# Optimization experiments

Hardware: AMD Instinct MI355X
Metric: run time of the kernel (lower is better)

The kernel has to match this reference:

```python
import jax, jax.numpy as jnp
import numpy as np

C = 256
EPS = 1e-5


def dwconv3x3(x, w):
    # x: [B,C,H,W], w: [C,1,3,3] depthwise (groups=C)
    return jax.lax.conv_general_dilated(
        x, w, window_strides=(1, 1), padding=((1, 1), (1, 1)),
        dimension_numbers=('NCHW', 'OIHW', 'NCHW'), feature_group_count=x.shape[1])


def bn(x, gamma, beta, mean, var):
    # inference-mode batchnorm over channel dim of NCHW
    inv = gamma * jax.lax.rsqrt(var + EPS)
    return x * inv[:, None, None] + (beta - mean * inv)[:, None, None]


def setup_inputs() -> dict:
    key = jax.random.key(0)
    ks = jax.random.split(key, 8)
    B, H, W = 32, 64, 64
    inp = {
        'x': jax.random.normal(ks[0], (B, C, H, W), jnp.float32),
        'edge_w': jax.random.normal(ks[1], (C, 1, 3, 3), jnp.float32) * 0.1,
        'edge_gamma': jnp.ones((C,), jnp.float32),
        'edge_beta': jnp.zeros((C,), jnp.float32),
        'edge_mean': jnp.zeros((C,), jnp.float32),
        'edge_var': jnp.ones((C,), jnp.float32),
        'fc1_w': jax.random.normal(ks[2], (C // 16, C), jnp.float32) * 0.05,
        'fc2_w': jax.random.normal(ks[3], (C, C // 16), jnp.float32) * 0.05,
        'fusion_w': jax.random.normal(ks[4], (C, 2 * C), jnp.float32) * 0.05,
        'fusion_b': jnp.zeros((C,), jnp.float32),
        'bn1_gamma': jnp.ones((C,), jnp.float32),
        'bn1_beta': jnp.zeros((C,), jnp.float32),
        'bn1_mean': jnp.zeros((C,), jnp.float32),
        'bn1_var': jnp.ones((C,), jnp.float32),
        'deform_w': jax.random.normal(ks[5], (C, 1, 3, 3), jnp.float32) * 0.1,
        'balance_w': jax.random.normal(ks[6], (C, C), jnp.float32) * 0.05,
        'balance_b': jnp.zeros((C,), jnp.float32),
        'bn2_gamma': jnp.ones((C,), jnp.float32),
        'bn2_beta': jnp.zeros((C,), jnp.float32),
        'bn2_mean': jnp.zeros((C,), jnp.float32),
        'bn2_var': jnp.ones((C,), jnp.float32),
    }
    return inp


def reference(x, edge_w, edge_gamma, edge_beta, edge_mean, edge_var,
              fc1_w, fc2_w, fusion_w, fusion_b,
              bn1_gamma, bn1_beta, bn1_mean, bn1_var,
              deform_w, balance_w, balance_b,
              bn2_gamma, bn2_beta, bn2_mean, bn2_var):
    # --- EdgeEnhancementAttention ---
    edge = jax.nn.relu(bn(dwconv3x3(x, edge_w), edge_gamma, edge_beta, edge_mean, edge_var))
    # SE channel attention
    avg = jnp.mean(x, axis=(2, 3))                       # [B,C]
    att = jax.nn.relu(avg @ fc1_w.T)                     # [B,C/16]
    att = jax.nn.sigmoid(att @ fc2_w.T)                  # [B,C]
    enhanced = x * att[:, :, None, None]
    fused = jnp.concatenate([enhanced, edge], axis=1)    # [B,2C,H,W]
    out = jnp.einsum('bchw,oc->bohw', fused, fusion_w) + fusion_b[None, :, None, None]
    out = bn(out, bn1_gamma, bn1_beta, bn1_mean, bn1_var)
    # --- DeformConv2d with zero offsets == plain depthwise 3x3 conv, no bias ---
    out = dwconv3x3(out, deform_w)
    # --- balance: 1x1 conv + BN, then gate by input ---
    out = jnp.einsum('bchw,oc->bohw', out, balance_w) + balance_b[None, :, None, None]
    out = bn(out, bn2_gamma, bn2_beta, bn2_mean, bn2_var)
    return out * x
```

## Files before the change

kernel.cpp:

```cpp
#include <hip/hip_runtime.h>
#include <math.h>

#define HW 4096
#define PLSTRIDE ((size_t)HW * 8)

typedef unsigned short ushort_t;
typedef short v8s __attribute__((ext_vector_type(8)));
typedef float v4f __attribute__((ext_vector_type(4)));

__device__ __forceinline__ float bf2f(ushort_t u) {
    union { unsigned int i; float f; } v; v.i = ((unsigned int)u) << 16; return v.f;
}
__device__ __forceinline__ ushort_t f2bf(float f) {
    unsigned int x = __float_as_uint(f);
    x += 0x7fffu + ((x >> 16) & 1u);
    return (ushort_t)(x >> 16);
}

__device__ __forceinline__ void gld16(const ushort_t* g, ushort_t* l) {
    __builtin_amdgcn_global_load_lds(
        (__attribute__((address_space(1))) void*)g,
        (__attribute__((address_space(3))) void*)l, 16, 0, 0);
}

__global__ __launch_bounds__(256) void k_consts(
    const float* eg, const float* ebt, const float* em, const float* ev,
    const float* fb,
    const float* g1, const float* b1, const float* m1, const float* v1,
    const float* balb,
    const float* g2, const float* b2, const float* m2, const float* v2,
    float* cbuf)
{
    int c = threadIdx.x;
    float iE = eg[c] * rsqrtf(ev[c] + 1e-5f);
    cbuf[c]       = iE;
    cbuf[256 + c] = ebt[c] - em[c] * iE;
    float i1 = g1[c] * rsqrtf(v1[c] + 1e-5f);
    cbuf[512 + c] = i1;
    cbuf[768 + c] = b1[c] - m1[c] * i1 + fb[c] * i1;
    float i2 = g2[c] * rsqrtf(v2[c] + 1e-5f);
    cbuf[1024 + c] = i2;
    cbuf[1280 + c] = b2[c] - m2[c] * i2 + balb[c] * i2;
}

__global__ __launch_bounds__(256) void k_wcopy(const float* fusw, const float* balw,
                                               ushort_t* fusw2b, ushort_t* balwb)
{
    int o = blockIdx.x, t = threadIdx.x;
    fusw2b[o * 256 + t] = f2bf(fusw[o * 512 + 256 + t]);
    balwb[o * 256 + t]  = f2bf(balw[o * 256 + t]);
}

__global__ __launch_bounds__(512) void k_edge(const float* x, const float* ew,
                                              const float* cbuf, ushort_t* A,
                                              float* avg)
{
    __shared__ __align__(16) ushort_t Xs[4096];
    __shared__ __align__(16) ushort_t Es[4096];
    int cg = blockIdx.x;
    int b = blockIdx.y;
    int t = threadIdx.x;
    int w = t & 63;
    int pl = t >> 6;
    int c = cg * 8 + pl;
    const float* px = x + ((size_t)(b * 256 + c)) * HW;
    ushort_t* AX = A + ((size_t)(b * 64 + cg)) * PLSTRIDE;
    ushort_t* AE = A + ((size_t)(b * 64 + 32 + cg)) * PLSTRIDE;
    float wt[9];
    #pragma unroll
    for (int k = 0; k < 9; ++k) wt[k] = ew[c * 9 + k];
    float sE = cbuf[c], cE = cbuf[256 + c];
    bool wl = (w > 0), wrr = (w < 63);

    float p0l = 0.f, p0c = 0.f, p0r = 0.f;
    float p1l, p1c, p1r;
    p1c = px[w];
    p1l = wl ? px[w - 1] : 0.f;
    p1r = wrr ? px[w + 1] : 0.f;
    float s = 0.f;
    for (int hb = 0; hb < 8; ++hb) {
        #pragma unroll
        for (int hi = 0; hi < 8; ++hi) {
            int h = hb * 8 + hi;
            float p2l, p2c, p2r;
            if (h < 63) {
                const float* row = px + (h + 1) * 64;
                p2c = row[w];
                p2l = wl ? row[w - 1] : 0.f;
                p2r = wrr ? row[w + 1] : 0.f;
            } else {
                p2l = p2c = p2r = 0.f;
            }
            float a = p0l * wt[0] + p0c * wt[1] + p0r * wt[2]
                    + p1l * wt[3] + p1c * wt[4] + p1r * wt[5]
                    + p2l * wt[6] + p2c * wt[7] + p2r * wt[8];
            s += p1c;
            float v = a * sE + cE;
            Es[hi * 512 + w * 8 + pl] = f2bf(v > 0.f ? v : 0.f);
            Xs[hi * 512 + w * 8 + pl] = f2bf(p1c);
            p0l = p1l; p0c = p1c; p0r = p1r;
            p1l = p2l; p1c = p2c; p1r = p2r;
        }
        __syncthreads();
        {
            int hwg = (hb * 8 + pl) * 64 + w;
            uint4 vx = *(const uint4*)&Xs[pl * 512 + w * 8];
            uint4 ve = *(const uint4*)&Es[pl * 512 + w * 8];
            *(uint4*)(AX + (size_t)hwg * 8) = vx;
            *(uint4*)(AE + (size_t)hwg * 8) = ve;
        }
        __syncthreads();
    }
    #pragma unroll
    for (int off = 32; off > 0; off >>= 1) s += __shfl_down(s, off, 64);
    if ((t & 63) == 0) avg[b * 256 + c] = s * (1.0f / HW);
}

__global__ __launch_bounds__(256) void k_sefold(const float* avg, const float* fc1,
                                                const float* fc2, const float* fusw,
                                                ushort_t* w1b)
{
    int b = blockIdx.x, t = threadIdx.x;
    __shared__ float av[256];
    __shared__ float hid[16];
    av[t] = avg[b * 256 + t];
    __syncthreads();
    if (t < 16) {
        float h = 0.f;
        for (int c = 0; c < 256; ++c) h += av[c] * fc1[t * 256 + c];
        hid[t] = h > 0.f ? h : 0.f;
    }
    __syncthreads();
    float a = 0.f;
    #pragma unroll
    for (int j = 0; j < 16; ++j) a += hid[j] * fc2[t * 16 + j];
    float att = 1.0f / (1.0f + expf(-a));
    ushort_t* wout = w1b + (size_t)b * 65536;
    for (int o = 0; o < 256; ++o)
        wout[o * 256 + t] = f2bf(fusw[o * 512 + t] * att);
}

__global__ __launch_bounds__(512, 4) void k_gemm1(ushort_t* __restrict__ A,
                                                  const ushort_t* __restrict__ w1b,
                                                  const ushort_t* __restrict__ fusw2b,
                                                  const float* __restrict__ cbuf)
{
    __shared__ __align__(16) ushort_t At[128 * 64];
    __shared__ __align__(16) ushort_t Bt[256 * 64];
    int bid = blockIdx.x;
    int orig = (bid & 7) * 128 + (bid >> 3);
    int b = orig >> 5;
    int hw0 = (orig & 31) * 128;
    int t = threadIdx.x;
    int lane = t & 63, wv = t >> 6;
    int quad = lane >> 4, l16 = lane & 15;
    int wr = wv >> 2, wc = wv & 3;
    int srow = lane >> 3, kch = lane & 7;

    v4f acc[4][4];
    #pragma unroll
    for (int i = 0; i < 4; ++i)
        #pragma unroll
        for (int j = 0; j < 4; ++j) acc[i][j] = (v4f){0.f, 0.f, 0.f, 0.f};

    for (int kb = 0; kb < 8; ++kb) {
        __syncthreads();
        #pragma unroll
        for (int r = 0; r < 2; ++r) {
            int mrow = wv * 8 + r * 64 + srow;
            int csw = kch ^ (mrow & 7);
            gld16(A + ((size_t)(b * 64 + kb * 8 + csw)) * PLSTRIDE
                    + (size_t)(hw0 + mrow) * 8,
                  &At[(wv * 8 + r * 64) * 64]);
        }
        #pragma unroll
        for (int r = 0; r < 4; ++r) {
            int orow = wv * 8 + r * 64 + srow;
            int kc2 = kch ^ (orow & 7);
            const ushort_t* bs = (kb < 4)
                ? (w1b + ((size_t)(b * 256 + orow)) * 256 + kb * 64 + kc2 * 8)
                : (fusw2b + ((size_t)orow) * 256 + (kb - 4) * 64 + kc2 * 8);
            gld16(bs, &Bt[(wv * 8 + r * 64) * 64]);
        }
        __syncthreads();
        #pragma unroll
        for (int ks2 = 0; ks2 < 2; ++ks2) {
            v8s afr[4], bfr[4];
            #pragma unroll
            for (int mt = 0; mt < 4; ++mt) {
                int ml = wr * 64 + mt * 16 + l16;
                int jj = (ks2 * 4 + quad) ^ (ml & 7);
                afr[mt] = *(const v8s*)(&At[ml * 64 + jj * 8]);
            }
            #pragma unroll
            for (int nt = 0; nt < 4; ++nt) {
                int ol = wc * 64 + nt * 16 + l16;
                int jj = (ks2 * 4 + quad) ^ (ol & 7);
                bfr[nt] = *(const v8s*)(&Bt[ol * 64 + jj * 8]);
            }
            #pragma unroll
            for (int mt = 0; mt < 4; ++mt)
                #pragma unroll
                for (int nt = 0; nt < 4; ++nt)
                    acc[mt][nt] = __builtin_amdgcn_mfma_f32_16x16x32_bf16(
                        afr[mt], bfr[nt], acc[mt][nt], 0, 0, 0);
        }
    }

    #pragma unroll
    for (int nt = 0; nt < 4; ++nt) {
        int o = wc * 64 + nt * 16 + l16;
        float s1 = cbuf[512 + o], c1 = cbuf[768 + o];
        ushort_t* op = A + ((size_t)(b * 64 + 32 + (o >> 3))) * PLSTRIDE + (o & 7);
        #pragma unroll
        for (int mt = 0; mt < 4; ++mt)
            #pragma unroll
            for (int r = 0; r < 4; ++r) {
                int m = hw0 + wr * 64 + mt * 16 + quad * 4 + r;
                op[(size_t)m * 8] = f2bf(acc[mt][nt][r] * s1 + c1);
            }
    }
}

__global__ __launch_bounds__(256) void k_dw2(ushort_t* __restrict__ A,
                                             const float* __restrict__ dfw)
{
    int t = threadIdx.x;
    int w = t & 63;
    int pl = t >> 6;
    int cg = blockIdx.x * 4 + pl;
    int b = blockIdx.y;
    int h0 = blockIdx.z * 32;
    const ushort_t* pE = A + ((size_t)(b * 64 + 32 + cg)) * PLSTRIDE;
    ushort_t* pX = A + ((size_t)(b * 64 + cg)) * PLSTRIDE;
    float wt[3][3][8];
    #pragma unroll
    for (int r = 0; r < 3; ++r)
        #pragma unroll
        for (int d = 0; d < 3; ++d)
            #pragma unroll
            for (int ch = 0; ch < 8; ++ch)
                wt[r][d][ch] = dfw[(cg * 8 + ch) * 9 + r * 3 + d];
    bool wl = (w > 0), wrr = (w < 63);

    uint4 rm, rc, rp;
    rm = (h0 > 0) ? *(const uint4*)(pE + (size_t)((h0 - 1) * 64 + w) * 8)
                  : (uint4){0u, 0u, 0u, 0u};
    rc = *(const uint4*)(pE + (size_t)(h0 * 64 + w) * 8);

#define DWROW(v, r) { \
    unsigned int cx0 = v.x, cx1 = v.y, cx2 = v.z, cx3 = v.w; \
    unsigned int lx0 = __shfl_up(cx0, 1, 64), lx1 = __shfl_up(cx1, 1, 64); \
    unsigned int lx2 = __shfl_up(cx2, 1, 64), lx3 = __shfl_up(cx3, 1, 64); \
    unsigned int rx0 = __shfl_down(cx0, 1, 64), rx1 = __shfl_down(cx1, 1, 64); \
    unsigned int rx2 = __shfl_down(cx2, 1, 64), rx3 = __shfl_down(cx3, 1, 64); \
    unsigned int cw[4] = { cx0, cx1, cx2, cx3 }; \
    unsigned int lw[4] = { lx0, lx1, lx2, lx3 }; \
    unsigned int rw[4] = { rx0, rx1, rx2, rx3 }; \
    _Pragma("unroll") for (int ch = 0; ch < 8; ++ch) { \
        float fC = bf2f((ch & 1) ? (ushort_t)(cw[ch >> 1] >> 16) \
                                 : (ushort_t)(cw[ch >> 1] & 0xffff)); \
        float fL = wl ? bf2f((ch & 1) ? (ushort_t)(lw[ch >> 1] >> 16) \
                                      : (ushort_t)(lw[ch >> 1] & 0xffff)) : 0.f; \
        float fR = wrr ? bf2f((ch & 1) ? (ushort_t)(rw[ch >> 1] >> 16) \
                                       : (ushort_t)(rw[ch >> 1] & 0xffff)) : 0.f; \
        acc[ch] += fL * wt[r][0][ch] + fC * wt[r][1][ch] + fR * wt[r][2][ch]; \
    } }

    for (int s = 0; s < 32; ++s) {
        int h = h0 + s;
        rp = (h + 1 < 64) ? *(const uint4*)(pE + (size_t)((h + 1) * 64 + w) * 8)
                          : (uint4){0u, 0u, 0u, 0u};
        float acc[8];
        #pragma unroll
        for (int ch = 0; ch < 8; ++ch) acc[ch] = 0.f;
        DWROW(rm, 0);
        DWROW(rc, 1);
        DWROW(rp, 2);
        uint4 ov;
        ov.x = (unsigned int)f2bf(acc[0]) | ((unsigned int)f2bf(acc[1]) << 16);
        ov.y = (unsigned int)f2bf(acc[2]) | ((unsigned int)f2bf(acc[3]) << 16);
        ov.z = (unsigned int)f2bf(acc[4]) | ((unsigned int)f2bf(acc[5]) << 16);
        ov.w = (unsigned int)f2bf(acc[6]) | ((unsigned int)f2bf(acc[7]) << 16);
        *(uint4*)(pX + (size_t)(h * 64 + w) * 8) = ov;
        rm = rc; rc = rp;
    }
#undef DWROW
}

__global__ __launch_bounds__(512, 4) void k_gemm2(ushort_t* __restrict__ A,
                                                  const ushort_t* __restrict__ balwb)
{
    __shared__ __align__(16) ushort_t At[128 * 64];
    __shared__ __align__(16) ushort_t Bt[256 * 64];
    int bid = blockIdx.x;
    int orig = (bid & 7) * 128 + (bid >> 3);
    int b = orig >> 5;
    int hw0 = (orig & 31) * 128;
    int t = threadIdx.x;
    int lane = t & 63, wv = t >> 6;
    int quad = lane >> 4, l16 = lane & 15;
    int wr = wv >> 2, wc = wv & 3;
    int srow = lane >> 3, kch = lane & 7;

    v4f acc[4][4];
    #pragma unroll
    for (int i = 0; i < 4; ++i)
        #pragma unroll
        for (int j = 0; j < 4; ++j) acc[i][j] = (v4f){0.f, 0.f, 0.f, 0.f};

    for (int kb = 0; kb < 4; ++kb) {
        __syncthreads();
        #pragma unroll
        for (int r = 0; r < 2; ++r) {
            int mrow = wv * 8 + r * 64 + srow;
            int csw = kch ^ (mrow & 7);
            gld16(A + ((size_t)(b * 64 + kb * 8 + csw)) * PLSTRIDE
                    + (size_t)(hw0 + mrow) * 8,
                  &At[(wv * 8 + r * 64) * 64]);
        }
        #pragma unroll
        for (int r = 0; r < 4; ++r) {
            int orow = wv * 8 + r * 64 + srow;
            int kc2 = kch ^ (orow & 7);
            gld16(balwb + ((size_t)orow) * 256 + kb * 64 + kc2 * 8,
                  &Bt[(wv * 8 + r * 64) * 64]);
        }
        __syncthreads();
        #pragma unroll
        for (int ks2 = 0; ks2 < 2; ++ks2) {
            v8s afr[4], bfr[4];
            #pragma unroll
            for (int mt = 0; mt < 4; ++mt) {
                int ml = wr * 64 + mt * 16 + l16;
                int jj = (ks2 * 4 + quad) ^ (ml & 7);
                afr[mt] = *(const v8s*)(&At[ml * 64 + jj * 8]);
            }
            #pragma unroll
            for (int nt = 0; nt < 4; ++nt) {
                int ol = wc * 64 + nt * 16 + l16;
                int jj = (ks2 * 4 + quad) ^ (ol & 7);
                bfr[nt] = *(const v8s*)(&Bt[ol * 64 + jj * 8]);
            }
            #pragma unroll
            for (int mt = 0; mt < 4; ++mt)
                #pragma unroll
                for (int nt = 0; nt < 4; ++nt)
                    acc[mt][nt] = __builtin_amdgcn_mfma_f32_16x16x32_bf16(
                        afr[mt], bfr[nt], acc[mt][nt], 0, 0, 0);
        }
    }

    #pragma unroll
    for (int nt = 0; nt < 4; ++nt) {
        int o = wc * 64 + nt * 16 + l16;
        ushort_t* op = A + ((size_t)(b * 64 + 32 + (o >> 3))) * PLSTRIDE + (o & 7);
        #pragma unroll
        for (int mt = 0; mt < 4; ++mt)
            #pragma unroll
            for (int r = 0; r < 4; ++r) {
                int m = hw0 + wr * 64 + mt * 16 + quad * 4 + r;
                op[(size_t)m * 8] = f2bf(acc[mt][nt][r]);
            }
    }
}

__global__ __launch_bounds__(256) void k_final(const ushort_t* A, const float* x,
                                               const float* cbuf, float* out)
{
    __shared__ float Lt[64 * 65];
    int bid = blockIdx.x;
    int b = bid >> 8;
    int rem = bid & 255;
    int hw0 = (rem >> 2) * 64;
    int c0 = (rem & 3) * 64;
    int t = threadIdx.x;
    #pragma unroll
    for (int r = 0; r < 2; ++r) {
        int idx = r * 256 + t;
        int cq = idx >> 6;
        int hwl = idx & 63;
        uint4 v = *(const uint4*)(A + ((size_t)(b * 64 + 32 + (c0 >> 3) + cq)) * PLSTRIDE
                                    + (size_t)(hw0 + hwl) * 8);
        unsigned int wd[4] = { v.x, v.y, v.z, v.w };
        #pragma unroll
        for (int j = 0; j < 8; ++j) {
            ushort_t u = (j & 1) ? (ushort_t)(wd[j >> 1] >> 16) : (ushort_t)(wd[j >> 1] & 0xffff);
            Lt[(cq * 8 + j) * 65 + hwl] = bf2f(u);
        }
    }
    __syncthreads();
    int hw_l = t & 63;
    int c_l0 = t >> 6;
    #pragma unroll
    for (int j = 0; j < 16; ++j) {
        int c_l = c_l0 * 16 + j;
        int c = c0 + c_l;
        float s2 = cbuf[1024 + c], c2 = cbuf[1280 + c];
        size_t g = ((size_t)b * 256 + c) * HW + hw0 + hw_l;
        float xv = x[g];
        out[g] = (Lt[c_l * 65 + hw_l] * s2 + c2) * xv;
    }
}

extern "C" void kernel_launch(void* const* d_in, const int* in_sizes, int n_in,
                              void* d_out, int out_size, void* d_ws, size_t ws_size,
                              hipStream_t stream)
{
    const float* x    = (const float*)d_in[0];
    const float* ew   = (const float*)d_in[1];
    const float* fc1  = (const float*)d_in[6];
    const float* fc2  = (const float*)d_in[7];
    const float* fusw = (const float*)d_in[8];
    const float* dfw  = (const float*)d_in[14];
    const float* balw = (const float*)d_in[15];
    float* out = (float*)d_out;

    char* ws = (char*)d_ws;
    ushort_t* A      = (ushort_t*)(ws);
    ushort_t* w1b    = (ushort_t*)(ws + 134217728);
    ushort_t* fusw2b = (ushort_t*)(ws + 138412032);
    ushort_t* balwb  = (ushort_t*)(ws + 138543104);
    float*    avg    = (float*)(ws + 138674176);
    float*    cbuf   = (float*)(ws + 138706944);

    k_consts<<<1, 256, 0, stream>>>((const float*)d_in[2], (const float*)d_in[3],
                                    (const float*)d_in[4], (const float*)d_in[5],
                                    (const float*)d_in[9],
                                    (const float*)d_in[10], (const float*)d_in[11],
                                    (const float*)d_in[12], (const float*)d_in[13],
                                    (const float*)d_in[16],
                                    (const float*)d_in[17], (const float*)d_in[18],
                                    (const float*)d_in[19], (const float*)d_in[20],
                                    cbuf);
    k_wcopy<<<256, 256, 0, stream>>>(fusw, balw, fusw2b, balwb);
    k_edge<<<dim3(32, 32), 512, 0, stream>>>(x, ew, cbuf, A, avg);
    k_sefold<<<32, 256, 0, stream>>>(avg, fc1, fc2, fusw, w1b);
    k_gemm1<<<1024, 512, 0, stream>>>(A, w1b, fusw2b, cbuf);
    k_dw2<<<dim3(8, 32, 2), 256, 0, stream>>>(A, dfw);
    k_gemm2<<<1024, 512, 0, stream>>>(A, balwb);
    k_final<<<8192, 256, 0, stream>>>(A, x, cbuf, out);
}
```

Before: 538.5 us.

## Vectorize edge kernel with float4 row loads, lane shuffles, and swizzled LDS transpose

The depthwise edge kernel now has each lane load float4 vectors covering four columns of three rows, taking the horizontal neighbours from adjacent lanes with shuffles instead of issuing scalar per-column loads. Results are packed as bf16 pairs into a 16-row XOR-swizzled LDS tile and transposed into the channel-interleaved layout with wider stores. Barriers drop from 16 to 8 per block. The goal is fewer global load instructions, fewer LDS bank conflicts and fewer synchronisations, at the cost of redundant vertical-neighbour loads and extra pack/unpack ALU work.

```diff
diff --git a/kernel.cpp b/kernel.cpp
--- a/kernel.cpp
+++ b/kernel.cpp
@@ -55,13 +55,16 @@
                                               const float* cbuf, ushort_t* A,
                                               float* avg)
 {
-    __shared__ __align__(16) ushort_t Xs[4096];
-    __shared__ __align__(16) ushort_t Es[4096];
+    __shared__ unsigned int Xs[16][8][32];
+    __shared__ unsigned int Es[16][8][32];
     int cg = blockIdx.x;
     int b = blockIdx.y;
     int t = threadIdx.x;
-    int w = t & 63;
+    int lane = t & 63;
     int pl = t >> 6;
+    int q = lane >> 4;
+    int l16 = lane & 15;
+    int w4 = l16 * 4;
     int c = cg * 8 + pl;
     const float* px = x + ((size_t)(b * 256 + c)) * HW;
     ushort_t* AX = A + ((size_t)(b * 64 + cg)) * PLSTRIDE;
@@ -70,44 +73,90 @@
     #pragma unroll
     for (int k = 0; k < 9; ++k) wt[k] = ew[c * 9 + k];
     float sE = cbuf[c], cE = cbuf[256 + c];
-    bool wl = (w > 0), wrr = (w < 63);
-
-    float p0l = 0.f, p0c = 0.f, p0r = 0.f;
-    float p1l, p1c, p1r;
-    p1c = px[w];
-    p1l = wl ? px[w - 1] : 0.f;
-    p1r = wrr ? px[w + 1] : 0.f;
+    bool wlz = (l16 > 0), wrz = (l16 < 15);
     float s = 0.f;
-    for (int hb = 0; hb < 8; ++hb) {
-        #pragma unroll
-        for (int hi = 0; hi < 8; ++hi) {
-            int h = hb * 8 + hi;
-            float p2l, p2c, p2r;
-            if (h < 63) {
-                const float* row = px + (h + 1) * 64;
-                p2c = row[w];
-                p2l = wl ? row[w - 1] : 0.f;
-                p2r = wrr ? row[w + 1] : 0.f;
-            } else {
-                p2l = p2c = p2r = 0.f;
-            }
-            float a = p0l * wt[0] + p0c * wt[1] + p0r * wt[2]
-                    + p1l * wt[3] + p1c * wt[4] + p1r * wt[5]
-                    + p2l * wt[6] + p2c * wt[7] + p2r * wt[8];
-            s += p1c;
-            float v = a * sE + cE;
-            Es[hi * 512 + w * 8 + pl] = f2bf(v > 0.f ? v : 0.f);
-            Xs[hi * 512 + w * 8 + pl] = f2bf(p1c);
-            p0l = p1l; p0c = p1c; p0r = p1r;
-            p1l = p2l; p1c = p2c; p1r = p2r;
+
+    for (int g4 = 0; g4 < 4; ++g4) {
+        #pragma unroll
+        for (int gi = 0; gi < 4; ++gi) {
+            int h = (g4 * 4 + gi) * 4 + q;
+            const float* rowp = px + h * 64 + w4;
+            float4 vc = *(const float4*)rowp;
+            float4 vm = (h > 0)  ? *(const float4*)(rowp - 64)
+                                 : make_float4(0.f, 0.f, 0.f, 0.f);
+            float4 vp = (h < 63) ? *(const float4*)(rowp + 64)
+                                 : make_float4(0.f, 0.f, 0.f, 0.f);
+            float lm_ = __shfl_up(vm.w, 1, 64);  float lm = wlz ? lm_ : 0.f;
+            float lc_ = __shfl_up(vc.w, 1, 64);  float lc = wlz ? lc_ : 0.f;
+            float lp_ = __shfl_up(vp.w, 1, 64);  float lp = wlz ? lp_ : 0.f;
+            float rm_ = __shfl_down(vm.x, 1, 64); float rm = wrz ? rm_ : 0.f;
+            float rc_ = __shfl_down(vc.x, 1, 64); float rc = wrz ? rc_ : 0.f;
+            float rp_ = __shfl_down(vp.x, 1, 64); float rp = wrz ? rp_ : 0.f;
+
+            float o0 = lm   * wt[0] + vm.x * wt[1] + vm.y * wt[2]
+                     + lc   * wt[3] + vc.x * wt[4] + vc.y * wt[5]
+                     + lp   * wt[6] + vp.x * wt[7] + vp.y * wt[8];
+            float o1 = vm.x * wt[0] + vm.y * wt[1] + vm.z * wt[2]
+                     + vc.x * wt[3] + vc.y * wt[4] + vc.z * wt[5]
+                     + vp.x * wt[6] + vp.y * wt[7] + vp.z * wt[8];
+            float o2 = vm.y * wt[0] + vm.z * wt[1] + vm.w * wt[2]
+                     + vc.y * wt[3] + vc.z * wt[4] + vc.w * wt[5]
+                     + vp.y * wt[6] + vp.z * wt[7] + vp.w * wt[8];
+            float o3 = vm.z * wt[0] + vm.w * wt[1] + rm   * wt[2]
+                     + vc.z * wt[3] + vc.w * wt[4] + rc   * wt[5]
+                     + vp.z * wt[6] + vp.w * wt[7] + rp   * wt[8];
+
+            float e0 = o0 * sE + cE; e0 = e0 > 0.f ? e0 : 0.f;
+            float e1 = o1 * sE + cE; e1 = e1 > 0.f ? e1 : 0.f;
+            float e2 = o2 * sE + cE; e2 = e2 > 0.f ? e2 : 0.f;
+            float e3 = o3 * sE + cE; e3 = e3 > 0.f ? e3 : 0.f;
+
+            unsigned int xlo = (unsigned int)f2bf(vc.x) | ((unsigned int)f2bf(vc.y) << 16);
+            unsigned int xhi = (unsigned int)f2bf(vc.z) | ((unsigned int)f2bf(vc.w) << 16);
+            unsigned int elo = (unsigned int)f2bf(e0) | ((unsigned int)f2bf(e1) << 16);
+            unsigned int ehi = (unsigned int)f2bf(e2) | ((unsigned int)f2bf(e3) << 16);
+
+            int r16 = gi * 4 + q;
+            int sz = r16 & 7;
+            Xs[r16][pl][(2 * l16) ^ sz]     = xlo;
+            Xs[r16][pl][(2 * l16 + 1) ^ sz] = xhi;
+            Es[r16][pl][(2 * l16) ^ sz]     = elo;
+            Es[r16][pl][(2 * l16 + 1) ^ sz] = ehi;
+            s += vc.x + vc.y + vc.z + vc.w;
         }
         __syncthreads();
         {
-            int hwg = (hb * 8 + pl) * 64 + w;
-            uint4 vx = *(const uint4*)&Xs[pl * 512 + w * 8];
-            uint4 ve = *(const uint4*)&Es[pl * 512 + w * 8];
-            *(uint4*)(AX + (size_t)hwg * 8) = vx;
-            *(uint4*)(AE + (size_t)hwg * 8) = ve;
+            int r16 = t >> 5;
+            int w2 = t & 31;
+            int sz = r16 & 7;
+            unsigned int ux[8], ue[8];
+            #pragma unroll
+            for (int ch = 0; ch < 8; ++ch) {
+                ux[ch] = Xs[r16][ch][w2 ^ sz];
+                ue[ch] = Es[r16][ch][w2 ^ sz];
+            }
+            uint4 x0, x1, e0v, e1v;
+            x0.x = (ux[0] & 0xffffu) | (ux[1] << 16);
+            x0.y = (ux[2] & 0xffffu) | (ux[3] << 16);
+            x0.z = (ux[4] & 0xffffu) | (ux[5] << 16);
+            x0.w = (ux[6] & 0xffffu) | (ux[7] << 16);
+            x1.x = (ux[0] >> 16) | (ux[1] & 0xffff0000u);
+            x1.y = (ux[2] >> 16) | (ux[3] & 0xffff0000u);
+            x1.z = (ux[4] >> 16) | (ux[5] & 0xffff0000u);
+            x1.w = (ux[6] >> 16) | (ux[7] & 0xffff0000u);
+            e0v.x = (ue[0] & 0xffffu) | (ue[1] << 16);
+            e0v.y = (ue[2] & 0xffffu) | (ue[3] << 16);
+            e0v.z = (ue[4] & 0xffffu) | (ue[5] << 16);
+            e0v.w = (ue[6] & 0xffffu) | (ue[7] << 16);
+            e1v.x = (ue[0] >> 16) | (ue[1] & 0xffff0000u);
+            e1v.y = (ue[2] >> 16) | (ue[3] & 0xffff0000u);
+            e1v.z = (ue[4] >> 16) | (ue[5] & 0xffff0000u);
+            e1v.w = (ue[6] >> 16) | (ue[7] & 0xffff0000u);
+            int hwg = (g4 * 16 + r16) * 64 + 2 * w2;
+            *(uint4*)(AX + (size_t)hwg * 8) = x0;
+            *(uint4*)(AX + (size_t)(hwg + 1) * 8) = x1;
+            *(uint4*)(AE + (size_t)hwg * 8) = e0v;
+            *(uint4*)(AE + (size_t)(hwg + 1) * 8) = e1v;
         }
         __syncthreads();
     }
```

Result: faster. 527.7 us (-2.0%).
